# Kernel optimization log

Hardware: AMD Instinct MI355X
Metric: run time of the kernel (lower is better)

## Reference

```python
import jax, jax.numpy as jnp
import numpy as np

N = 131072        # number of points
S = 16384         # number of groups (segments)
D_IN = 256        # fea_dims[0]
NUM_RF = 1024     # random-feature width
D_OUT = 128       # fea_dims[1] (embedding dim)
_INV_SQRT2 = 1.0 / np.sqrt(2.0).astype(np.float32)
_INV_SQRT2PI = 1.0 / np.sqrt(2.0 * np.pi).astype(np.float32)


def setup_inputs() -> dict:
    key = jax.random.key(0)
    k1, k2, k3, k4, k5, k6 = jax.random.split(key, 6)
    X = jax.random.normal(k1, (N, D_IN), dtype=jnp.float32)
    # balanced group assignment (guarantees no empty segment -> no inf/nan)
    X_idx = jax.random.permutation(k2, jnp.arange(N, dtype=jnp.int64) % S)
    W1_mu = jax.random.normal(k3, (NUM_RF, D_IN), dtype=jnp.float32) * 0.05
    W1_var = jax.random.uniform(k4, (NUM_RF, D_IN), dtype=jnp.float32) * 0.01 + 1e-4
    W2_mu = jax.random.normal(k5, (D_OUT, NUM_RF), dtype=jnp.float32) * 0.05
    W2_var = jax.random.uniform(k6, (D_OUT, NUM_RF), dtype=jnp.float32) * 0.01 + 1e-4
    return {"X": X, "X_idx": X_idx, "W1_mu": W1_mu, "W1_var": W1_var,
            "W2_mu": W2_mu, "W2_var": W2_var}


def _vb_linear(m, v, W_mu, W_var):
    # Variational Bayes linear layer: propagate mean/variance through
    # independent Gaussian weights W ~ N(W_mu, W_var).
    mo = m @ W_mu.T                                   # [N, out]
    if v is None:
        vo = (m * m) @ W_var.T
    else:
        vo = v @ (W_mu * W_mu).T + (m * m + v) @ W_var.T
    return mo, vo


def _relu_moments(mu, var):
    # Exact first/second moments of ReLU of a Gaussian N(mu, var).
    s = jnp.sqrt(var + 1e-8)
    z = mu / s
    Phi = 0.5 * (1.0 + jax.scipy.special.erf(z * _INV_SQRT2))
    phi = jnp.exp(-0.5 * z * z) * _INV_SQRT2PI
    m_out = mu * Phi + s * phi
    e_y2 = (mu * mu + var) * Phi + mu * s * phi
    v_out = jnp.maximum(e_y2 - m_out * m_out, 1e-6)
    return m_out, v_out


def reference(X, X_idx, W1_mu, W1_var, W2_mu, W2_var):
    # DGP-RF block: D_IN -> NUM_RF (ReLU moments) -> D_OUT
    m, v = _vb_linear(X, None, W1_mu, W1_var)         # [N, NUM_RF]
    m, v = _relu_moments(m, v)
    out_means, out_vars = _vb_linear(m, v, W2_mu, W2_var)  # [N, D_OUT]
    # Precision-weighted aggregation over X_idx groups (Gaussian product)
    prec = 1.0 / out_vars                              # [N, D_OUT]
    embedd_vars = 1.0 / jax.ops.segment_sum(prec, X_idx, num_segments=S)
    embedd_means = jax.ops.segment_sum(prec * out_means, X_idx, num_segments=S)
    embedd_means = embedd_means * embedd_vars          # [S, D_OUT]
    return embedd_means, embedd_vars
```

## Files before the change

kernel.cpp:

```cpp
#include <hip/hip_runtime.h>


#define NPTS   131072
#define SGRP   16384
#define DIN    256
#define NRF    1024
#define DOUT   128
#define MT     64
#define NWG    (NPTS / MT)

#define XLD    264
#define XQLD   264
#define TMLD   72
#define TVLD   72

typedef unsigned short ushort_t;
typedef unsigned char  uchar_t;
typedef __attribute__((ext_vector_type(8))) short bf16x8;
typedef __attribute__((ext_vector_type(4))) float f32x4;
typedef __attribute__((ext_vector_type(4))) float f32x4v;

__device__ __forceinline__ unsigned short f2bf(float f) {
  unsigned u = __float_as_uint(f);
  u += 0x7fffu + ((u >> 16) & 1u);
  return (unsigned short)(u >> 16);
}

template <bool HI>
__device__ __forceinline__ unsigned cvt2_fp8(float a, float b, unsigned old) {
#if __has_builtin(__builtin_amdgcn_cvt_pk_fp8_f32)
  return __builtin_amdgcn_cvt_pk_fp8_f32(a, b, old, HI);
#else
  auto enc = [](float x) -> unsigned {
    if (!(x > 0.00097656f)) return 0u;
    if (x >= 448.f) return 0x7Eu;
    union { float f; unsigned u; } v; v.f = x;
    int e = (int)(v.u >> 23) - 127;
    if (e < -6) { int n = (int)(x * 512.f + 0.5f); return (unsigned)n; }
    v.u += 0x0007FFFFu + ((v.u >> 20) & 1u);
    e = (int)(v.u >> 23) - 127;
    if (e > 8) return 0x7Eu;
    return (unsigned)(((e + 7) << 3) | ((v.u >> 20) & 7u));
  };
  unsigned p = (enc(a) | (enc(b) << 8));
  return HI ? ((old & 0x0000ffffu) | (p << 16)) : ((old & 0xffff0000u) | p);
#endif
}

__device__ __forceinline__ float fast_rcp(float x) {
#if __has_builtin(__builtin_amdgcn_rcpf)
  return __builtin_amdgcn_rcpf(x);
#else
  return 1.0f / x;
#endif
}
__device__ __forceinline__ float fast_rsq(float x) {
#if __has_builtin(__builtin_amdgcn_rsqf)
  return __builtin_amdgcn_rsqf(x);
#else
  return rsqrtf(x);
#endif
}
__device__ __forceinline__ float fast_exp2(float x) {
#if __has_builtin(__builtin_amdgcn_exp2f)
  return __builtin_amdgcn_exp2f(x);
#else
  return exp2f(x);
#endif
}

__device__ __forceinline__ void relu_moments(float mu, float v,
                                             float& mo, float& vo) {
  float vpe = v + 1e-8f;
  float rsq = fast_rsq(vpe);
  float s   = vpe * rsq;
  float z   = mu * rsq;
  float E   = fast_exp2(-0.7213475204444817f * z * z);
  float x   = 0.70710678118654752f * fabsf(z);
  float t   = fast_rcp(fmaf(0.3275911f, x, 1.0f));
  float poly = t * fmaf(t, fmaf(t, fmaf(t, fmaf(t, 1.061405429f, -1.453152027f),
                                        1.421413741f), -0.284496736f), 0.254829592f);
  float q   = 0.5f * poly * E;
  float Phi = (z >= 0.0f) ? (1.0f - q) : q;
  float phi = 0.3989422804014327f * E;
  float sphi = s * phi;
  mo = fmaf(mu, Phi, sphi);
  float ey2 = fmaf(fmaf(mu, mu, v), Phi, mu * sphi);
  vo = fmaxf(fmaf(-mo, mo, ey2), 1e-6f);
}

__global__ void detect_idx_kernel(const unsigned* __restrict__ raw,
                                  int* __restrict__ flag) {
  __shared__ int any_nz;
  if (threadIdx.x == 0) any_nz = 0;
  __syncthreads();
  if (raw[2 * threadIdx.x + 1] != 0u) atomicOr(&any_nz, 1);
  __syncthreads();
  if (threadIdx.x == 0) *flag = (any_nz == 0) ? 1 : 0;
}

__global__ __launch_bounds__(256) void convert_kernel(
    const float* __restrict__ W1mu, const float* __restrict__ W1var,
    const float* __restrict__ W2mu, const float* __restrict__ W2var,
    ushort_t* __restrict__ w1mu_bf, uchar_t* __restrict__ w1var8,
    ushort_t* __restrict__ w2mu_bf, uchar_t* __restrict__ w2b8,
    uchar_t* __restrict__ w2var8) {
  int i4 = (blockIdx.x * 256 + threadIdx.x) * 4;
  {
    f32x4v m = *(const f32x4v*)(W1mu + i4);
    ushort4 b; b.x = f2bf(m[0]); b.y = f2bf(m[1]); b.z = f2bf(m[2]); b.w = f2bf(m[3]);
    *(ushort4*)(w1mu_bf + i4) = b;
    f32x4v v = *(const f32x4v*)(W1var + i4);
    unsigned p = cvt2_fp8<false>(v[0] * 256.f, v[1] * 256.f, 0u);
    p = cvt2_fp8<true>(v[2] * 256.f, v[3] * 256.f, p);
    *(unsigned*)(w1var8 + i4) = p;
  }
  if (i4 < NRF * DOUT) {
    f32x4v m = *(const f32x4v*)(W2mu + i4);
    f32x4v v = *(const f32x4v*)(W2var + i4);
    ushort4 b; b.x = f2bf(m[0]); b.y = f2bf(m[1]); b.z = f2bf(m[2]); b.w = f2bf(m[3]);
    *(ushort4*)(w2mu_bf + i4) = b;
    unsigned pb = cvt2_fp8<false>(fmaf(m[0], m[0], v[0]) * 256.f,
                                  fmaf(m[1], m[1], v[1]) * 256.f, 0u);
    pb = cvt2_fp8<true>(fmaf(m[2], m[2], v[2]) * 256.f,
                        fmaf(m[3], m[3], v[3]) * 256.f, pb);
    *(unsigned*)(w2b8 + i4) = pb;
    unsigned pv = cvt2_fp8<false>(v[0] * 256.f, v[1] * 256.f, 0u);
    pv = cvt2_fp8<true>(v[2] * 256.f, v[3] * 256.f, pv);
    *(unsigned*)(w2var8 + i4) = pv;
  }
}

__global__ __launch_bounds__(256, 2) void fused_kernel(
    const float* __restrict__ X,
    const unsigned* __restrict__ Xidx_raw,
    const ushort_t* __restrict__ W1mu, const uchar_t* __restrict__ W1var8,
    const ushort_t* __restrict__ W2mu, const uchar_t* __restrict__ W2b8,
    const uchar_t* __restrict__ W2var8,
    const int* __restrict__ flag64,
    float* __restrict__ acc_means, float* __restrict__ acc_vars) {
  __shared__ ushort_t Xb[MT * XLD];
  __shared__ uchar_t  Xq8[MT * XQLD];
  __shared__ ushort_t Tm[MT * TMLD];
  __shared__ uchar_t  Tv8[MT * TVLD];
  __shared__ uchar_t  T38[MT * TVLD];
  __shared__ int sidx[MT];

  const int tid = threadIdx.x;
  const int p0  = blockIdx.x * MT;
  const int is64 = *flag64;

  if (tid < MT) {
    int p = p0 + tid;
    sidx[tid] = (int)(is64 ? Xidx_raw[2 * (size_t)p] : Xidx_raw[p]);
  }
#pragma unroll
  for (int i = 0; i < 16; ++i) {
    int idx4 = i * 256 + tid;
    int row  = idx4 >> 6;
    int c4   = idx4 & 63;
    f32x4v xv = *(const f32x4v*)(X + (size_t)(p0 + row) * DIN + c4 * 4);
    ushort4 b;
    b.x = f2bf(xv[0]); b.y = f2bf(xv[1]); b.z = f2bf(xv[2]); b.w = f2bf(xv[3]);
    *(ushort4*)(Xb + row * XLD + c4 * 4) = b;
    unsigned q = cvt2_fp8<false>(xv[0] * xv[0], xv[1] * xv[1], 0u);
    q = cvt2_fp8<true>(xv[2] * xv[2], xv[3] * xv[3], q);
    *(unsigned*)(Xq8 + row * XQLD + c4 * 4) = q;
  }
  __syncthreads();

  const int lane = tid & 63;
  const int wave = tid >> 6;
  const int l16  = lane & 15;
  const int quad = lane >> 4;
  const int qoff = quad * 8;

  const int nrow0 = (wave * 2 + 0) * 16 + l16;
  const int nrow1 = (wave * 2 + 1) * 16 + l16;

  f32x4 acc_mo[4][2], acc_vo[4][2];
#pragma unroll
  for (int mt = 0; mt < 4; ++mt)
#pragma unroll
    for (int j = 0; j < 2; ++j) {
      acc_mo[mt][j] = (f32x4){0.f, 0.f, 0.f, 0.f};
      acc_vo[mt][j] = (f32x4){0.f, 0.f, 0.f, 0.f};
    }

#pragma unroll 1
  for (int c = 0; c < 16; ++c) {
    const ushort_t* w1m = W1mu  + (size_t)(c * 64 + wave * 16 + l16) * DIN + qoff;
    const uchar_t*  w1v = W1var8 + (size_t)(c * 64 + wave * 16 + l16) * DIN + qoff;
    bf16x8 bmu[8]; long long bvr[8];
#pragma unroll
    for (int k = 0; k < 8; ++k) {
      bmu[k] = *(const bf16x8*)(w1m + k * 32);
      bvr[k] = *(const long long*)(w1v + k * 32);
    }
    f32x4 am[4], av[4];
#pragma unroll
    for (int mt = 0; mt < 4; ++mt) {
      am[mt] = (f32x4){0.f, 0.f, 0.f, 0.f};
      av[mt] = (f32x4){0.f, 0.f, 0.f, 0.f};
    }
#pragma unroll
    for (int k = 0; k < 8; ++k) {
#pragma unroll
      for (int mt = 0; mt < 4; ++mt) {
        bf16x8 ax = *(const bf16x8*)(Xb + (mt * 16 + l16) * XLD + k * 32 + qoff);
        long long aq = *(const long long*)(Xq8 + (mt * 16 + l16) * XQLD + k * 32 + qoff);
        am[mt] = __builtin_amdgcn_mfma_f32_16x16x32_bf16(ax, bmu[k], am[mt], 0, 0, 0);
        av[mt] = __builtin_amdgcn_mfma_f32_16x16x32_fp8_fp8(aq, bvr[k], av[mt], 0, 0, 0);
      }
    }

    const ushort_t* w2m0 = W2mu + (size_t)nrow0 * NRF + c * 64 + qoff;
    const ushort_t* w2m1 = W2mu + (size_t)nrow1 * NRF + c * 64 + qoff;
    const uchar_t* w2b0 = W2b8 + (size_t)nrow0 * NRF + c * 64 + qoff;
    const uchar_t* w2b1 = W2b8 + (size_t)nrow1 * NRF + c * 64 + qoff;
    const uchar_t* w2v0 = W2var8 + (size_t)nrow0 * NRF + c * 64 + qoff;
    const uchar_t* w2v1 = W2var8 + (size_t)nrow1 * NRF + c * 64 + qoff;
    bf16x8 b2m[2][2]; long long b2b[2][2], b2v[2][2];
#pragma unroll
    for (int k2 = 0; k2 < 2; ++k2) {
      b2m[0][k2] = *(const bf16x8*)(w2m0 + k2 * 32);
      b2m[1][k2] = *(const bf16x8*)(w2m1 + k2 * 32);
      b2b[0][k2] = *(const long long*)(w2b0 + k2 * 32);
      b2b[1][k2] = *(const long long*)(w2b1 + k2 * 32);
      b2v[0][k2] = *(const long long*)(w2v0 + k2 * 32);
      b2v[1][k2] = *(const long long*)(w2v1 + k2 * 32);
    }

    __syncthreads();

    const int col = wave * 16 + l16;
#pragma unroll
    for (int mt = 0; mt < 4; ++mt) {
#pragma unroll
      for (int r = 0; r < 4; ++r) {
        float mo, vo;
        relu_moments(am[mt][r], av[mt][r] * 0.00390625f, mo, vo);
        int row = mt * 16 + quad * 4 + r;
        Tm[row * TMLD + col] = f2bf(mo);
        Tv8[row * TVLD + col] = (uchar_t)(cvt2_fp8<false>(vo, vo, 0u) & 0xffu);
        T38[row * TVLD + col] = (uchar_t)(cvt2_fp8<false>(mo * mo, mo * mo, 0u) & 0xffu);
      }
    }
    __syncthreads();

#pragma unroll
    for (int k2 = 0; k2 < 2; ++k2) {
#pragma unroll
      for (int mt = 0; mt < 4; ++mt) {
        int ar = mt * 16 + l16;
        bf16x8 fam = *(const bf16x8*)(Tm + ar * TMLD + k2 * 32 + qoff);
        long long fav = *(const long long*)(Tv8 + ar * TVLD + k2 * 32 + qoff);
        long long f3  = *(const long long*)(T38 + ar * TVLD + k2 * 32 + qoff);
        acc_mo[mt][0] = __builtin_amdgcn_mfma_f32_16x16x32_bf16(fam, b2m[0][k2], acc_mo[mt][0], 0, 0, 0);
        acc_mo[mt][1] = __builtin_amdgcn_mfma_f32_16x16x32_bf16(fam, b2m[1][k2], acc_mo[mt][1], 0, 0, 0);
        acc_vo[mt][0] = __builtin_amdgcn_mfma_f32_16x16x32_fp8_fp8(fav, b2b[0][k2], acc_vo[mt][0], 0, 0, 0);
        acc_vo[mt][1] = __builtin_amdgcn_mfma_f32_16x16x32_fp8_fp8(fav, b2b[1][k2], acc_vo[mt][1], 0, 0, 0);
        acc_vo[mt][0] = __builtin_amdgcn_mfma_f32_16x16x32_fp8_fp8(f3, b2v[0][k2], acc_vo[mt][0], 0, 0, 0);
        acc_vo[mt][1] = __builtin_amdgcn_mfma_f32_16x16x32_fp8_fp8(f3, b2v[1][k2], acc_vo[mt][1], 0, 0, 0);
      }
    }
  }

#pragma unroll
  for (int mt = 0; mt < 4; ++mt)
#pragma unroll
    for (int j = 0; j < 2; ++j) {
      int dim = (wave * 2 + j) * 16 + l16;
#pragma unroll
      for (int r = 0; r < 4; ++r) {
        int prow = mt * 16 + quad * 4 + r;
        float mo = acc_mo[mt][j][r];
        float vo = fmaf(acc_vo[mt][j][r], 0.00390625f, 1e-6f);
        float prec = fast_rcp(vo);
        size_t o = (size_t)sidx[prow] * DOUT + dim;
        unsafeAtomicAdd(acc_means + o, prec * mo);
        unsafeAtomicAdd(acc_vars + o, prec);
      }
    }
}

__global__ __launch_bounds__(256) void finalize_kernel(float* __restrict__ means,
                                                       float* __restrict__ vars) {
  int i = blockIdx.x * 256 + threadIdx.x;
  float p  = vars[i];
  float pm = means[i];
  float var = 1.0f / p;
  means[i] = pm * var;
  vars[i]  = var;
}

extern "C" void kernel_launch(void* const* d_in, const int* in_sizes, int n_in,
                              void* d_out, int out_size, void* d_ws, size_t ws_size,
                              hipStream_t stream) {
  const float*    X     = (const float*)d_in[0];
  const unsigned* Xidx  = (const unsigned*)d_in[1];
  const float*    W1mu  = (const float*)d_in[2];
  const float*    W1var = (const float*)d_in[3];
  const float*    W2mu  = (const float*)d_in[4];
  const float*    W2var = (const float*)d_in[5];
  float* out = (float*)d_out;

  ushort_t* w1mu_bf = (ushort_t*)d_ws;
  uchar_t*  w1var8  = (uchar_t*)(w1mu_bf + NRF * DIN);
  ushort_t* w2mu_bf = (ushort_t*)(w1var8 + NRF * DIN);
  uchar_t*  w2b8    = (uchar_t*)(w2mu_bf + NRF * DOUT);
  uchar_t*  w2var8  = w2b8 + NRF * DOUT;
  int* flag = (int*)(w2var8 + NRF * DOUT);

  (void)hipMemsetAsync(d_out, 0, (size_t)out_size * sizeof(float), stream);
  detect_idx_kernel<<<1, 256, 0, stream>>>(Xidx, flag);
  convert_kernel<<<(NRF * DIN) / 4 / 256, 256, 0, stream>>>(
      W1mu, W1var, W2mu, W2var, w1mu_bf, w1var8, w2mu_bf, w2b8, w2var8);
  fused_kernel<<<NWG, 256, 0, stream>>>(
      X, Xidx, w1mu_bf, w1var8, w2mu_bf, w2b8, w2var8, flag,
      out, out + (size_t)SGRP * DOUT);
  finalize_kernel<<<(SGRP * DOUT) / 256, 256, 0, stream>>>(
      out, out + (size_t)SGRP * DOUT);
}
```

Before: 653.4 us.

## Software-pipeline first-layer MFMA of next chunk with ReLU-moment epilogue

Restructures the chunk loop so the first-layer GEMM for chunk c+1 is issued before the ReLU-moment math and LDS stores of chunk c. The MFMA work can then overlap the transcendental VALU work and LDS traffic within the same wave. The cost is a second set of accumulators (am2/av2), which raises register pressure and may reduce occupancy or cause spills.

```diff
diff --git a/kernel.cpp b/kernel.cpp
--- a/kernel.cpp
+++ b/kernel.cpp
@@ -187,17 +187,17 @@
       acc_vo[mt][j] = (f32x4){0.f, 0.f, 0.f, 0.f};
     }
 
-#pragma unroll 1
-  for (int c = 0; c < 16; ++c) {
-    const ushort_t* w1m = W1mu  + (size_t)(c * 64 + wave * 16 + l16) * DIN + qoff;
-    const uchar_t*  w1v = W1var8 + (size_t)(c * 64 + wave * 16 + l16) * DIN + qoff;
+  f32x4 am[4], av[4], am2[4], av2[4];
+
+  {
+    const ushort_t* w1m = W1mu  + (size_t)(wave * 16 + l16) * DIN + qoff;
+    const uchar_t*  w1v = W1var8 + (size_t)(wave * 16 + l16) * DIN + qoff;
     bf16x8 bmu[8]; long long bvr[8];
 #pragma unroll
     for (int k = 0; k < 8; ++k) {
       bmu[k] = *(const bf16x8*)(w1m + k * 32);
       bvr[k] = *(const long long*)(w1v + k * 32);
     }
-    f32x4 am[4], av[4];
 #pragma unroll
     for (int mt = 0; mt < 4; ++mt) {
       am[mt] = (f32x4){0.f, 0.f, 0.f, 0.f};
@@ -213,7 +213,10 @@
         av[mt] = __builtin_amdgcn_mfma_f32_16x16x32_fp8_fp8(aq, bvr[k], av[mt], 0, 0, 0);
       }
     }
-
+  }
+
+#pragma unroll 1
+  for (int c = 0; c < 16; ++c) {
     const ushort_t* w2m0 = W2mu + (size_t)nrow0 * NRF + c * 64 + qoff;
     const ushort_t* w2m1 = W2mu + (size_t)nrow1 * NRF + c * 64 + qoff;
     const uchar_t* w2b0 = W2b8 + (size_t)nrow0 * NRF + c * 64 + qoff;
@@ -232,6 +235,32 @@
     }
 
     __syncthreads();
+
+    if (c < 15) {
+      const ushort_t* w1m = W1mu  + (size_t)((c + 1) * 64 + wave * 16 + l16) * DIN + qoff;
+      const uchar_t*  w1v = W1var8 + (size_t)((c + 1) * 64 + wave * 16 + l16) * DIN + qoff;
+      bf16x8 bmu[8]; long long bvr[8];
+#pragma unroll
+      for (int k = 0; k < 8; ++k) {
+        bmu[k] = *(const bf16x8*)(w1m + k * 32);
+        bvr[k] = *(const long long*)(w1v + k * 32);
+      }
+#pragma unroll
+      for (int mt = 0; mt < 4; ++mt) {
+        am2[mt] = (f32x4){0.f, 0.f, 0.f, 0.f};
+        av2[mt] = (f32x4){0.f, 0.f, 0.f, 0.f};
+      }
+#pragma unroll
+      for (int k = 0; k < 8; ++k) {
+#pragma unroll
+        for (int mt = 0; mt < 4; ++mt) {
+          bf16x8 ax = *(const bf16x8*)(Xb + (mt * 16 + l16) * XLD + k * 32 + qoff);
+          long long aq = *(const long long*)(Xq8 + (mt * 16 + l16) * XQLD + k * 32 + qoff);
+          am2[mt] = __builtin_amdgcn_mfma_f32_16x16x32_bf16(ax, bmu[k], am2[mt], 0, 0, 0);
+          av2[mt] = __builtin_amdgcn_mfma_f32_16x16x32_fp8_fp8(aq, bvr[k], av2[mt], 0, 0, 0);
+        }
+      }
+    }
 
     const int col = wave * 16 + l16;
 #pragma unroll
@@ -264,6 +293,12 @@
         acc_vo[mt][1] = __builtin_amdgcn_mfma_f32_16x16x32_fp8_fp8(f3, b2v[1][k2], acc_vo[mt][1], 0, 0, 0);
       }
     }
+
+#pragma unroll
+    for (int mt = 0; mt < 4; ++mt) {
+      am[mt] = am2[mt];
+      av[mt] = av2[mt];
+    }
   }
 
 #pragma unroll
```

Result: slower. 756.6 us (+15.8%).

## Switch fused MLP to 32x32x16 MFMA tiles with transposed operand roles

Applied to the files above, without the earlier changes.

Replaces the 16x16x32 MFMA tiling with 32x32x16 MFMA instructions and reassigns waves to a 2x2 grid of point blocks and RF/output blocks. The first GEMM now puts weights in the A operand and points in B, so the ReLU-moment results can be packed and written to LDS as 4-element vector stores instead of byte and short scatters. The aim is fewer MFMA issues, more operand reuse per instruction and cheaper LDS writes. It costs more live registers, since 16 weight fragments per operand type are held per chunk, which may lower occupancy.

```diff
diff --git a/kernel.cpp b/kernel.cpp
--- a/kernel.cpp
+++ b/kernel.cpp
@@ -17,7 +17,7 @@
 typedef unsigned short ushort_t;
 typedef unsigned char  uchar_t;
 typedef __attribute__((ext_vector_type(8))) short bf16x8;
-typedef __attribute__((ext_vector_type(4))) float f32x4;
+typedef __attribute__((ext_vector_type(16))) float f32x16;
 typedef __attribute__((ext_vector_type(4))) float f32x4v;
 
 __device__ __forceinline__ unsigned short f2bf(float f) {
@@ -169,119 +169,106 @@
   }
   __syncthreads();
 
-  const int lane = tid & 63;
-  const int wave = tid >> 6;
-  const int l16  = lane & 15;
-  const int quad = lane >> 4;
-  const int qoff = quad * 8;
-
-  const int nrow0 = (wave * 2 + 0) * 16 + l16;
-  const int nrow1 = (wave * 2 + 1) * 16 + l16;
-
-  f32x4 acc_mo[4][2], acc_vo[4][2];
-#pragma unroll
-  for (int mt = 0; mt < 4; ++mt)
-#pragma unroll
-    for (int j = 0; j < 2; ++j) {
-      acc_mo[mt][j] = (f32x4){0.f, 0.f, 0.f, 0.f};
-      acc_vo[mt][j] = (f32x4){0.f, 0.f, 0.f, 0.f};
-    }
+  const int lane  = tid & 63;
+  const int wave  = tid >> 6;
+  const int col32 = lane & 31;
+  const int khalf = lane >> 5;
+
+  const int rfblk = wave & 1;
+  const int ptblk = wave >> 1;
+  const int d0    = (wave & 1) * 2;
+  const int ptA   = ptblk * 32 + col32;
+
+  f32x16 acc_mo[2], acc_vo[2];
+#pragma unroll
+  for (int d = 0; d < 2; ++d)
+#pragma unroll
+    for (int i = 0; i < 16; ++i) { acc_mo[d][i] = 0.f; acc_vo[d][i] = 0.f; }
 
 #pragma unroll 1
   for (int c = 0; c < 16; ++c) {
-    const ushort_t* w1m = W1mu  + (size_t)(c * 64 + wave * 16 + l16) * DIN + qoff;
-    const uchar_t*  w1v = W1var8 + (size_t)(c * 64 + wave * 16 + l16) * DIN + qoff;
-    bf16x8 bmu[8]; long long bvr[8];
-#pragma unroll
-    for (int k = 0; k < 8; ++k) {
-      bmu[k] = *(const bf16x8*)(w1m + k * 32);
-      bvr[k] = *(const long long*)(w1v + k * 32);
-    }
-    f32x4 am[4], av[4];
-#pragma unroll
-    for (int mt = 0; mt < 4; ++mt) {
-      am[mt] = (f32x4){0.f, 0.f, 0.f, 0.f};
-      av[mt] = (f32x4){0.f, 0.f, 0.f, 0.f};
-    }
-#pragma unroll
-    for (int k = 0; k < 8; ++k) {
-#pragma unroll
-      for (int mt = 0; mt < 4; ++mt) {
-        bf16x8 ax = *(const bf16x8*)(Xb + (mt * 16 + l16) * XLD + k * 32 + qoff);
-        long long aq = *(const long long*)(Xq8 + (mt * 16 + l16) * XQLD + k * 32 + qoff);
-        am[mt] = __builtin_amdgcn_mfma_f32_16x16x32_bf16(ax, bmu[k], am[mt], 0, 0, 0);
-        av[mt] = __builtin_amdgcn_mfma_f32_16x16x32_fp8_fp8(aq, bvr[k], av[mt], 0, 0, 0);
+    const ushort_t* w1m = W1mu   + (size_t)(c * 64 + rfblk * 32 + col32) * DIN + khalf * 8;
+    const uchar_t*  w1v = W1var8 + (size_t)(c * 64 + rfblk * 32 + col32) * DIN + khalf * 8;
+    bf16x8 w1f[16]; long long w1q[16];
+#pragma unroll
+    for (int k = 0; k < 16; ++k) {
+      w1f[k] = *(const bf16x8*)(w1m + k * 16);
+      w1q[k] = *(const long long*)(w1v + k * 16);
+    }
+    f32x16 am, av;
+#pragma unroll
+    for (int i = 0; i < 16; ++i) { am[i] = 0.f; av[i] = 0.f; }
+#pragma unroll
+    for (int k = 0; k < 16; ++k) {
+      bf16x8 bx = *(const bf16x8*)(Xb + ptA * XLD + k * 16 + khalf * 8);
+      long long bq = *(const long long*)(Xq8 + ptA * XQLD + k * 16 + khalf * 8);
+      am = __builtin_amdgcn_mfma_f32_32x32x16_bf16(w1f[k], bx, am, 0, 0, 0);
+      av = __builtin_amdgcn_mfma_f32_32x32x16_fp8_fp8(w1q[k], bq, av, 0, 0, 0);
+    }
+
+    bf16x8 b2m[4][2]; long long b2b[4][2], b2v[4][2];
+#pragma unroll
+    for (int d = 0; d < 2; ++d) {
+      size_t wb = (size_t)((d0 + d) * 32 + col32) * NRF + c * 64 + khalf * 8;
+#pragma unroll
+      for (int ks = 0; ks < 4; ++ks) {
+        b2m[ks][d] = *(const bf16x8*)(W2mu + wb + ks * 16);
+        b2b[ks][d] = *(const long long*)(W2b8 + wb + ks * 16);
+        b2v[ks][d] = *(const long long*)(W2var8 + wb + ks * 16);
       }
     }
 
-    const ushort_t* w2m0 = W2mu + (size_t)nrow0 * NRF + c * 64 + qoff;
-    const ushort_t* w2m1 = W2mu + (size_t)nrow1 * NRF + c * 64 + qoff;
-    const uchar_t* w2b0 = W2b8 + (size_t)nrow0 * NRF + c * 64 + qoff;
-    const uchar_t* w2b1 = W2b8 + (size_t)nrow1 * NRF + c * 64 + qoff;
-    const uchar_t* w2v0 = W2var8 + (size_t)nrow0 * NRF + c * 64 + qoff;
-    const uchar_t* w2v1 = W2var8 + (size_t)nrow1 * NRF + c * 64 + qoff;
-    bf16x8 b2m[2][2]; long long b2b[2][2], b2v[2][2];
-#pragma unroll
-    for (int k2 = 0; k2 < 2; ++k2) {
-      b2m[0][k2] = *(const bf16x8*)(w2m0 + k2 * 32);
-      b2m[1][k2] = *(const bf16x8*)(w2m1 + k2 * 32);
-      b2b[0][k2] = *(const long long*)(w2b0 + k2 * 32);
-      b2b[1][k2] = *(const long long*)(w2b1 + k2 * 32);
-      b2v[0][k2] = *(const long long*)(w2v0 + k2 * 32);
-      b2v[1][k2] = *(const long long*)(w2v1 + k2 * 32);
-    }
-
     __syncthreads();
 
-    const int col = wave * 16 + l16;
-#pragma unroll
-    for (int mt = 0; mt < 4; ++mt) {
-#pragma unroll
-      for (int r = 0; r < 4; ++r) {
-        float mo, vo;
-        relu_moments(am[mt][r], av[mt][r] * 0.00390625f, mo, vo);
-        int row = mt * 16 + quad * 4 + r;
-        Tm[row * TMLD + col] = f2bf(mo);
-        Tv8[row * TVLD + col] = (uchar_t)(cvt2_fp8<false>(vo, vo, 0u) & 0xffu);
-        T38[row * TVLD + col] = (uchar_t)(cvt2_fp8<false>(mo * mo, mo * mo, 0u) & 0xffu);
+    const int rfb = rfblk * 32 + 4 * khalf;
+#pragma unroll
+    for (int qi = 0; qi < 4; ++qi) {
+      float mo0, vo0, mo1, vo1, mo2, vo2, mo3, vo3;
+      relu_moments(am[4 * qi + 0], av[4 * qi + 0] * 0.00390625f, mo0, vo0);
+      relu_moments(am[4 * qi + 1], av[4 * qi + 1] * 0.00390625f, mo1, vo1);
+      relu_moments(am[4 * qi + 2], av[4 * qi + 2] * 0.00390625f, mo2, vo2);
+      relu_moments(am[4 * qi + 3], av[4 * qi + 3] * 0.00390625f, mo3, vo3);
+      unsigned lo = (unsigned)f2bf(mo0) | ((unsigned)f2bf(mo1) << 16);
+      unsigned hi = (unsigned)f2bf(mo2) | ((unsigned)f2bf(mo3) << 16);
+      unsigned long long tmq = (unsigned long long)lo | ((unsigned long long)hi << 32);
+      *(unsigned long long*)(Tm + ptA * TMLD + rfb + 8 * qi) = tmq;
+      unsigned tvq = cvt2_fp8<false>(vo0, vo1, 0u);
+      tvq = cvt2_fp8<true>(vo2, vo3, tvq);
+      *(unsigned*)(Tv8 + ptA * TVLD + rfb + 8 * qi) = tvq;
+      unsigned t3q = cvt2_fp8<false>(mo0 * mo0, mo1 * mo1, 0u);
+      t3q = cvt2_fp8<true>(mo2 * mo2, mo3 * mo3, t3q);
+      *(unsigned*)(T38 + ptA * TVLD + rfb + 8 * qi) = t3q;
+    }
+    __syncthreads();
+
+#pragma unroll
+    for (int ks = 0; ks < 4; ++ks) {
+      bf16x8 fam = *(const bf16x8*)(Tm + ptA * TMLD + ks * 16 + khalf * 8);
+      long long fav = *(const long long*)(Tv8 + ptA * TVLD + ks * 16 + khalf * 8);
+      long long f3  = *(const long long*)(T38 + ptA * TVLD + ks * 16 + khalf * 8);
+#pragma unroll
+      for (int d = 0; d < 2; ++d) {
+        acc_mo[d] = __builtin_amdgcn_mfma_f32_32x32x16_bf16(fam, b2m[ks][d], acc_mo[d], 0, 0, 0);
+        acc_vo[d] = __builtin_amdgcn_mfma_f32_32x32x16_fp8_fp8(fav, b2b[ks][d], acc_vo[d], 0, 0, 0);
+        acc_vo[d] = __builtin_amdgcn_mfma_f32_32x32x16_fp8_fp8(f3, b2v[ks][d], acc_vo[d], 0, 0, 0);
       }
     }
-    __syncthreads();
-
-#pragma unroll
-    for (int k2 = 0; k2 < 2; ++k2) {
-#pragma unroll
-      for (int mt = 0; mt < 4; ++mt) {
-        int ar = mt * 16 + l16;
-        bf16x8 fam = *(const bf16x8*)(Tm + ar * TMLD + k2 * 32 + qoff);
-        long long fav = *(const long long*)(Tv8 + ar * TVLD + k2 * 32 + qoff);
-        long long f3  = *(const long long*)(T38 + ar * TVLD + k2 * 32 + qoff);
-        acc_mo[mt][0] = __builtin_amdgcn_mfma_f32_16x16x32_bf16(fam, b2m[0][k2], acc_mo[mt][0], 0, 0, 0);
-        acc_mo[mt][1] = __builtin_amdgcn_mfma_f32_16x16x32_bf16(fam, b2m[1][k2], acc_mo[mt][1], 0, 0, 0);
-        acc_vo[mt][0] = __builtin_amdgcn_mfma_f32_16x16x32_fp8_fp8(fav, b2b[0][k2], acc_vo[mt][0], 0, 0, 0);
-        acc_vo[mt][1] = __builtin_amdgcn_mfma_f32_16x16x32_fp8_fp8(fav, b2b[1][k2], acc_vo[mt][1], 0, 0, 0);
-        acc_vo[mt][0] = __builtin_amdgcn_mfma_f32_16x16x32_fp8_fp8(f3, b2v[0][k2], acc_vo[mt][0], 0, 0, 0);
-        acc_vo[mt][1] = __builtin_amdgcn_mfma_f32_16x16x32_fp8_fp8(f3, b2v[1][k2], acc_vo[mt][1], 0, 0, 0);
-      }
-    }
-  }
-
-#pragma unroll
-  for (int mt = 0; mt < 4; ++mt)
-#pragma unroll
-    for (int j = 0; j < 2; ++j) {
-      int dim = (wave * 2 + j) * 16 + l16;
-#pragma unroll
-      for (int r = 0; r < 4; ++r) {
-        int prow = mt * 16 + quad * 4 + r;
-        float mo = acc_mo[mt][j][r];
-        float vo = fmaf(acc_vo[mt][j][r], 0.00390625f, 1e-6f);
-        float prec = fast_rcp(vo);
-        size_t o = (size_t)sidx[prow] * DOUT + dim;
-        unsafeAtomicAdd(acc_means + o, prec * mo);
-        unsafeAtomicAdd(acc_vars + o, prec);
-      }
-    }
+  }
+
+#pragma unroll
+  for (int d = 0; d < 2; ++d) {
+    int dout = (d0 + d) * 32 + col32;
+#pragma unroll
+    for (int rg = 0; rg < 16; ++rg) {
+      int pt = ptblk * 32 + (rg & 3) + 8 * (rg >> 2) + 4 * khalf;
+      float mo = acc_mo[d][rg];
+      float vo = fmaf(acc_vo[d][rg], 0.00390625f, 1e-6f);
+      float prec = fast_rcp(vo);
+      size_t o = (size_t)sidx[pt] * DOUT + dout;
+      unsafeAtomicAdd(acc_means + o, prec * mo);
+      unsafeAtomicAdd(acc_vars + o, prec);
+    }
+  }
 }
 
 __global__ __launch_bounds__(256) void finalize_kernel(float* __restrict__ means,
```

Result: slower. 1.024 ms (+56.7%).

## Warp-specialize fused kernel into producer and consumer waves with double-buffered LDS

Applied to the files above, without the earlier changes.

Doubles the block to 512 threads and splits the waves into two roles. Producer waves compute the first-layer GEMM and ReLU moments into double-buffered LDS tiles. Consumer waves run the second-layer GEMM and the atomic segment accumulation. The goal is to overlap stage-1 and stage-2 MFMA work and the W2 loads across chunks instead of serialising them with two barriers per chunk. The cost is one block per CU instead of two and extra LDS. A single __syncthreads per chunk now guards both the buffer handoff and its reuse, so the handoff timing is tight.

```diff
diff --git a/kernel.cpp b/kernel.cpp
--- a/kernel.cpp
+++ b/kernel.cpp
@@ -131,7 +131,7 @@
   }
 }
 
-__global__ __launch_bounds__(256, 2) void fused_kernel(
+__global__ __launch_bounds__(512, 1) void fused_kernel(
     const float* __restrict__ X,
     const unsigned* __restrict__ Xidx_raw,
     const ushort_t* __restrict__ W1mu, const uchar_t* __restrict__ W1var8,
@@ -141,9 +141,9 @@
     float* __restrict__ acc_means, float* __restrict__ acc_vars) {
   __shared__ ushort_t Xb[MT * XLD];
   __shared__ uchar_t  Xq8[MT * XQLD];
-  __shared__ ushort_t Tm[MT * TMLD];
-  __shared__ uchar_t  Tv8[MT * TVLD];
-  __shared__ uchar_t  T38[MT * TVLD];
+  __shared__ ushort_t Tm[2][MT * TMLD];
+  __shared__ uchar_t  Tv8[2][MT * TVLD];
+  __shared__ uchar_t  T38[2][MT * TVLD];
   __shared__ int sidx[MT];
 
   const int tid = threadIdx.x;
@@ -155,8 +155,8 @@
     sidx[tid] = (int)(is64 ? Xidx_raw[2 * (size_t)p] : Xidx_raw[p]);
   }
 #pragma unroll
-  for (int i = 0; i < 16; ++i) {
-    int idx4 = i * 256 + tid;
+  for (int i = 0; i < 8; ++i) {
+    int idx4 = i * 512 + tid;
     int row  = idx4 >> 6;
     int c4   = idx4 & 63;
     f32x4v xv = *(const f32x4v*)(X + (size_t)(p0 + row) * DIN + c4 * 4);
@@ -171,117 +171,125 @@
 
   const int lane = tid & 63;
   const int wave = tid >> 6;
+  const int role = wave & 1;
+  const int wid  = wave >> 1;
   const int l16  = lane & 15;
   const int quad = lane >> 4;
   const int qoff = quad * 8;
 
-  const int nrow0 = (wave * 2 + 0) * 16 + l16;
-  const int nrow1 = (wave * 2 + 1) * 16 + l16;
-
-  f32x4 acc_mo[4][2], acc_vo[4][2];
-#pragma unroll
-  for (int mt = 0; mt < 4; ++mt)
-#pragma unroll
-    for (int j = 0; j < 2; ++j) {
-      acc_mo[mt][j] = (f32x4){0.f, 0.f, 0.f, 0.f};
-      acc_vo[mt][j] = (f32x4){0.f, 0.f, 0.f, 0.f};
+  if (role == 0) {
+    const int col = wid * 16 + l16;
+#pragma unroll 1
+    for (int c = 0; c < 16; ++c) {
+      const ushort_t* w1m = W1mu  + (size_t)(c * 64 + wid * 16 + l16) * DIN + qoff;
+      const uchar_t*  w1v = W1var8 + (size_t)(c * 64 + wid * 16 + l16) * DIN + qoff;
+      bf16x8 bmu[8]; long long bvr[8];
+#pragma unroll
+      for (int k = 0; k < 8; ++k) {
+        bmu[k] = *(const bf16x8*)(w1m + k * 32);
+        bvr[k] = *(const long long*)(w1v + k * 32);
+      }
+      f32x4 am[4], av[4];
+#pragma unroll
+      for (int mt = 0; mt < 4; ++mt) {
+        am[mt] = (f32x4){0.f, 0.f, 0.f, 0.f};
+        av[mt] = (f32x4){0.f, 0.f, 0.f, 0.f};
+      }
+#pragma unroll
+      for (int k = 0; k < 8; ++k) {
+#pragma unroll
+        for (int mt = 0; mt < 4; ++mt) {
+          bf16x8 ax = *(const bf16x8*)(Xb + (mt * 16 + l16) * XLD + k * 32 + qoff);
+          long long aq = *(const long long*)(Xq8 + (mt * 16 + l16) * XQLD + k * 32 + qoff);
+          am[mt] = __builtin_amdgcn_mfma_f32_16x16x32_bf16(ax, bmu[k], am[mt], 0, 0, 0);
+          av[mt] = __builtin_amdgcn_mfma_f32_16x16x32_fp8_fp8(aq, bvr[k], av[mt], 0, 0, 0);
+        }
+      }
+      const int buf = c & 1;
+#pragma unroll
+      for (int mt = 0; mt < 4; ++mt) {
+#pragma unroll
+        for (int r = 0; r < 4; ++r) {
+          float mo, vo;
+          relu_moments(am[mt][r], av[mt][r] * 0.00390625f, mo, vo);
+          int row = mt * 16 + quad * 4 + r;
+          Tm[buf][row * TMLD + col] = f2bf(mo);
+          Tv8[buf][row * TVLD + col] = (uchar_t)(cvt2_fp8<false>(vo, vo, 0u) & 0xffu);
+          T38[buf][row * TVLD + col] = (uchar_t)(cvt2_fp8<false>(mo * mo, mo * mo, 0u) & 0xffu);
+        }
+      }
+      __syncthreads();
     }
+  } else {
+    const int nrow0 = (wid * 2 + 0) * 16 + l16;
+    const int nrow1 = (wid * 2 + 1) * 16 + l16;
+
+    f32x4 acc_mo[4][2], acc_vo[4][2];
+#pragma unroll
+    for (int mt = 0; mt < 4; ++mt)
+#pragma unroll
+      for (int j = 0; j < 2; ++j) {
+        acc_mo[mt][j] = (f32x4){0.f, 0.f, 0.f, 0.f};
+        acc_vo[mt][j] = (f32x4){0.f, 0.f, 0.f, 0.f};
+      }
 
 #pragma unroll 1
-  for (int c = 0; c < 16; ++c) {
-    const ushort_t* w1m = W1mu  + (size_t)(c * 64 + wave * 16 + l16) * DIN + qoff;
-    const uchar_t*  w1v = W1var8 + (size_t)(c * 64 + wave * 16 + l16) * DIN + qoff;
-    bf16x8 bmu[8]; long long bvr[8];
-#pragma unroll
-    for (int k = 0; k < 8; ++k) {
-      bmu[k] = *(const bf16x8*)(w1m + k * 32);
-      bvr[k] = *(const long long*)(w1v + k * 32);
+    for (int c = 0; c < 16; ++c) {
+      const ushort_t* w2m0 = W2mu + (size_t)nrow0 * NRF + c * 64 + qoff;
+      const ushort_t* w2m1 = W2mu + (size_t)nrow1 * NRF + c * 64 + qoff;
+      const uchar_t* w2b0 = W2b8 + (size_t)nrow0 * NRF + c * 64 + qoff;
+      const uchar_t* w2b1 = W2b8 + (size_t)nrow1 * NRF + c * 64 + qoff;
+      const uchar_t* w2v0 = W2var8 + (size_t)nrow0 * NRF + c * 64 + qoff;
+      const uchar_t* w2v1 = W2var8 + (size_t)nrow1 * NRF + c * 64 + qoff;
+      bf16x8 b2m[2][2]; long long b2b[2][2], b2v[2][2];
+#pragma unroll
+      for (int k2 = 0; k2 < 2; ++k2) {
+        b2m[0][k2] = *(const bf16x8*)(w2m0 + k2 * 32);
+        b2m[1][k2] = *(const bf16x8*)(w2m1 + k2 * 32);
+        b2b[0][k2] = *(const long long*)(w2b0 + k2 * 32);
+        b2b[1][k2] = *(const long long*)(w2b1 + k2 * 32);
+        b2v[0][k2] = *(const long long*)(w2v0 + k2 * 32);
+        b2v[1][k2] = *(const long long*)(w2v1 + k2 * 32);
+      }
+
+      __syncthreads();
+
+      const int buf = c & 1;
+#pragma unroll
+      for (int k2 = 0; k2 < 2; ++k2) {
+#pragma unroll
+        for (int mt = 0; mt < 4; ++mt) {
+          int ar = mt * 16 + l16;
+          bf16x8 fam = *(const bf16x8*)(Tm[buf] + ar * TMLD + k2 * 32 + qoff);
+          long long fav = *(const long long*)(Tv8[buf] + ar * TVLD + k2 * 32 + qoff);
+          long long f3  = *(const long long*)(T38[buf] + ar * TVLD + k2 * 32 + qoff);
+          acc_mo[mt][0] = __builtin_amdgcn_mfma_f32_16x16x32_bf16(fam, b2m[0][k2], acc_mo[mt][0], 0, 0, 0);
+          acc_mo[mt][1] = __builtin_amdgcn_mfma_f32_16x16x32_bf16(fam, b2m[1][k2], acc_mo[mt][1], 0, 0, 0);
+          acc_vo[mt][0] = __builtin_amdgcn_mfma_f32_16x16x32_fp8_fp8(fav, b2b[0][k2], acc_vo[mt][0], 0, 0, 0);
+          acc_vo[mt][1] = __builtin_amdgcn_mfma_f32_16x16x32_fp8_fp8(fav, b2b[1][k2], acc_vo[mt][1], 0, 0, 0);
+          acc_vo[mt][0] = __builtin_amdgcn_mfma_f32_16x16x32_fp8_fp8(f3, b2v[0][k2], acc_vo[mt][0], 0, 0, 0);
+          acc_vo[mt][1] = __builtin_amdgcn_mfma_f32_16x16x32_fp8_fp8(f3, b2v[1][k2], acc_vo[mt][1], 0, 0, 0);
+        }
+      }
     }
-    f32x4 am[4], av[4];
-#pragma unroll
-    for (int mt = 0; mt < 4; ++mt) {
-      am[mt] = (f32x4){0.f, 0.f, 0.f, 0.f};
-      av[mt] = (f32x4){0.f, 0.f, 0.f, 0.f};
-    }
-#pragma unroll
-    for (int k = 0; k < 8; ++k) {
-#pragma unroll
-      for (int mt = 0; mt < 4; ++mt) {
-        bf16x8 ax = *(const bf16x8*)(Xb + (mt * 16 + l16) * XLD + k * 32 + qoff);
-        long long aq = *(const long long*)(Xq8 + (mt * 16 + l16) * XQLD + k * 32 + qoff);
-        am[mt] = __builtin_amdgcn_mfma_f32_16x16x32_bf16(ax, bmu[k], am[mt], 0, 0, 0);
-        av[mt] = __builtin_amdgcn_mfma_f32_16x16x32_fp8_fp8(aq, bvr[k], av[mt], 0, 0, 0);
-      }
-    }
-
-    const ushort_t* w2m0 = W2mu + (size_t)nrow0 * NRF + c * 64 + qoff;
-    const ushort_t* w2m1 = W2mu + (size_t)nrow1 * NRF + c * 64 + qoff;
-    const uchar_t* w2b0 = W2b8 + (size_t)nrow0 * NRF + c * 64 + qoff;
-    const uchar_t* w2b1 = W2b8 + (size_t)nrow1 * NRF + c * 64 + qoff;
-    const uchar_t* w2v0 = W2var8 + (size_t)nrow0 * NRF + c * 64 + qoff;
-    const uchar_t* w2v1 = W2var8 + (size_t)nrow1 * NRF + c * 64 + qoff;
-    bf16x8 b2m[2][2]; long long b2b[2][2], b2v[2][2];
-#pragma unroll
-    for (int k2 = 0; k2 < 2; ++k2) {
-      b2m[0][k2] = *(const bf16x8*)(w2m0 + k2 * 32);
-      b2m[1][k2] = *(const bf16x8*)(w2m1 + k2 * 32);
-      b2b[0][k2] = *(const long long*)(w2b0 + k2 * 32);
-      b2b[1][k2] = *(const long long*)(w2b1 + k2 * 32);
-      b2v[0][k2] = *(const long long*)(w2v0 + k2 * 32);
-      b2v[1][k2] = *(const long long*)(w2v1 + k2 * 32);
-    }
-
-    __syncthreads();
-
-    const int col = wave * 16 + l16;
-#pragma unroll
-    for (int mt = 0; mt < 4; ++mt) {
-#pragma unroll
-      for (int r = 0; r < 4; ++r) {
-        float mo, vo;
-        relu_moments(am[mt][r], av[mt][r] * 0.00390625f, mo, vo);
-        int row = mt * 16 + quad * 4 + r;
-        Tm[row * TMLD + col] = f2bf(mo);
-        Tv8[row * TVLD + col] = (uchar_t)(cvt2_fp8<false>(vo, vo, 0u) & 0xffu);
-        T38[row * TVLD + col] = (uchar_t)(cvt2_fp8<false>(mo * mo, mo * mo, 0u) & 0xffu);
-      }
-    }
-    __syncthreads();
-
-#pragma unroll
-    for (int k2 = 0; k2 < 2; ++k2) {
-#pragma unroll
-      for (int mt = 0; mt < 4; ++mt) {
-        int ar = mt * 16 + l16;
-        bf16x8 fam = *(const bf16x8*)(Tm + ar * TMLD + k2 * 32 + qoff);
-        long long fav = *(const long long*)(Tv8 + ar * TVLD + k2 * 32 + qoff);
-        long long f3  = *(const long long*)(T38 + ar * TVLD + k2 * 32 + qoff);
-        acc_mo[mt][0] = __builtin_amdgcn_mfma_f32_16x16x32_bf16(fam, b2m[0][k2], acc_mo[mt][0], 0, 0, 0);
-        acc_mo[mt][1] = __builtin_amdgcn_mfma_f32_16x16x32_bf16(fam, b2m[1][k2], acc_mo[mt][1], 0, 0, 0);
-        acc_vo[mt][0] = __builtin_amdgcn_mfma_f32_16x16x32_fp8_fp8(fav, b2b[0][k2], acc_vo[mt][0], 0, 0, 0);
-        acc_vo[mt][1] = __builtin_amdgcn_mfma_f32_16x16x32_fp8_fp8(fav, b2b[1][k2], acc_vo[mt][1], 0, 0, 0);
-        acc_vo[mt][0] = __builtin_amdgcn_mfma_f32_16x16x32_fp8_fp8(f3, b2v[0][k2], acc_vo[mt][0], 0, 0, 0);
-        acc_vo[mt][1] = __builtin_amdgcn_mfma_f32_16x16x32_fp8_fp8(f3, b2v[1][k2], acc_vo[mt][1], 0, 0, 0);
-      }
-    }
-  }
-
-#pragma unroll
-  for (int mt = 0; mt < 4; ++mt)
-#pragma unroll
-    for (int j = 0; j < 2; ++j) {
-      int dim = (wave * 2 + j) * 16 + l16;
-#pragma unroll
-      for (int r = 0; r < 4; ++r) {
-        int prow = mt * 16 + quad * 4 + r;
-        float mo = acc_mo[mt][j][r];
-        float vo = fmaf(acc_vo[mt][j][r], 0.00390625f, 1e-6f);
-        float prec = fast_rcp(vo);
-        size_t o = (size_t)sidx[prow] * DOUT + dim;
-        unsafeAtomicAdd(acc_means + o, prec * mo);
-        unsafeAtomicAdd(acc_vars + o, prec);
-      }
-    }
+
+#pragma unroll
+    for (int mt = 0; mt < 4; ++mt)
+#pragma unroll
+      for (int j = 0; j < 2; ++j) {
+        int dim = (wid * 2 + j) * 16 + l16;
+#pragma unroll
+        for (int r = 0; r < 4; ++r) {
+          int prow = mt * 16 + quad * 4 + r;
+          float mo = acc_mo[mt][j][r];
+          float vo = fmaf(acc_vo[mt][j][r], 0.00390625f, 1e-6f);
+          float prec = fast_rcp(vo);
+          size_t o = (size_t)sidx[prow] * DOUT + dim;
+          unsafeAtomicAdd(acc_means + o, prec * mo);
+          unsafeAtomicAdd(acc_vars + o, prec);
+        }
+      }
+  }
 }
 
 __global__ __launch_bounds__(256) void finalize_kernel(float* __restrict__ means,
@@ -316,7 +324,7 @@
   detect_idx_kernel<<<1, 256, 0, stream>>>(Xidx, flag);
   convert_kernel<<<(NRF * DIN) / 4 / 256, 256, 0, stream>>>(
       W1mu, W1var, W2mu, W2var, w1mu_bf, w1var8, w2mu_bf, w2b8, w2var8);
-  fused_kernel<<<NWG, 256, 0, stream>>>(
+  fused_kernel<<<NWG, 512, 0, stream>>>(
       X, Xidx, w1mu_bf, w1var8, w2mu_bf, w2b8, w2var8, flag,
       out, out + (size_t)SGRP * DOUT);
   finalize_kernel<<<(SGRP * DOUT) / 256, 256, 0, stream>>>(
```

Measured after the change: 959.9 us. +46.9%, slower.
